# Kernel optimization log

Hardware: AMD Instinct MI355X
Metric: run time of the kernel (lower is better)

## Reference

```python
import jax, jax.numpy as jnp
import numpy as np

B_SZ = 16
IN_CH = 4
OUT_CH = 256          # d_model
KSIZE = 16
STRIDE = 8
L_IN = 20000
D_STATE = 128
EXPAND = 2
D_INNER = EXPAND * OUT_CH            # 512
HEADDIM = 64
NHEADS = D_INNER // HEADDIM          # 8
D_CONV = 4
NGROUPS = 1
L_CONV = (L_IN - KSIZE) // STRIDE + 1  # 2499
FLAT = STRIDE * L_CONV                 # 19992 == Config.INPUT_LENGTH
CHUNK = 128
DN = ('NCH', 'OIH', 'NCH')


def setup_inputs() -> dict:
    key = jax.random.key(0)
    ks = jax.random.split(key, 20)
    r = lambda i, shape, s=0.02: jax.random.normal(ks[i], shape, jnp.float32) * s
    return {
        'x': jax.random.normal(ks[0], (B_SZ, IN_CH, L_IN), jnp.float32),
        'conv_w': r(1, (OUT_CH, IN_CH, KSIZE), 0.1),
        'conv_b': r(2, (OUT_CH,), 0.1),
        'bn_w': jnp.ones((OUT_CH,), jnp.float32),
        'bn_b': jnp.zeros((OUT_CH,), jnp.float32),
        'in_proj_w': r(3, (2 * D_INNER + 2 * NGROUPS * D_STATE + NHEADS, OUT_CH)),
        'conv1d_w': r(4, (D_INNER + 2 * NGROUPS * D_STATE, 1, D_CONV), 0.2),
        'conv1d_b': r(5, (D_INNER + 2 * NGROUPS * D_STATE,), 0.1),
        'dt_bias': jnp.linspace(-4.0, -1.0, NHEADS, dtype=jnp.float32),
        'A_log': jnp.log(jnp.arange(1, NHEADS + 1, dtype=jnp.float32)),
        'D': r(6, (NHEADS,), 0.5) + 1.0,
        'norm_w': jnp.ones((D_INNER,), jnp.float32),
        'out_proj_w': r(7, (OUT_CH, D_INNER)),
        'conv1_w': r(8, (STRIDE, OUT_CH, KSIZE), 0.05),
        'conv1_b': r(9, (STRIDE,), 0.1),
        'w1': r(10, (512, FLAT)), 'b1': jnp.zeros((512,), jnp.float32),
        'w2': r(11, (256, 512), 0.05), 'b2': jnp.zeros((256,), jnp.float32),
        'w3': r(12, (64, 256), 0.05), 'b3': jnp.zeros((64,), jnp.float32),
        'w4': r(13, (1, 64), 0.05), 'b4': jnp.zeros((1,), jnp.float32),
    }


def _segsum(a):
    # a: [..., q] -> [..., q, q]; entry (i,j) = sum_{k=j+1..i} a_k on lower triangle
    q = a.shape[-1]
    cs = jnp.cumsum(a, axis=-1)
    seg = cs[..., :, None] - cs[..., None, :]
    mask = jnp.tril(jnp.ones((q, q), dtype=bool))
    return jnp.where(mask, seg, -jnp.inf)


def _ssd(xw, dA, Bm, Cm, chunk):
    # Chunked SSD (Mamba2): xw = dt-weighted inputs [b,l,h,p]; dA = dt*A [b,l,h];
    # Bm, Cm: [b,l,n]. Causal; zero-padding at the tail cannot affect y[:, :l].
    b, l, h, p = xw.shape
    n = Bm.shape[-1]
    pad = (-l) % chunk
    xw = jnp.pad(xw, ((0, 0), (0, pad), (0, 0), (0, 0)))
    dA = jnp.pad(dA, ((0, 0), (0, pad), (0, 0)))
    Bm = jnp.pad(Bm, ((0, 0), (0, pad), (0, 0)))
    Cm = jnp.pad(Cm, ((0, 0), (0, pad), (0, 0)))
    c = (l + pad) // chunk
    xw = xw.reshape(b, c, chunk, h, p)
    dA = dA.reshape(b, c, chunk, h).transpose(0, 3, 1, 2)   # [b,h,c,q]
    Bm = Bm.reshape(b, c, chunk, n)
    Cm = Cm.reshape(b, c, chunk, n)
    Acs = jnp.cumsum(dA, axis=-1)                            # [b,h,c,q]
    Ldiag = jnp.exp(_segsum(dA))                             # [b,h,c,q,q]
    Ydiag = jnp.einsum('bcln,bcsn,bhcls,bcshp->bclhp', Cm, Bm, Ldiag, xw)
    decay_states = jnp.exp(Acs[..., -1:] - Acs)              # [b,h,c,q]
    states = jnp.einsum('bcln,bhcl,bclhp->bchpn', Bm, decay_states, xw)
    chunk_decay = jnp.exp(Acs[..., -1])                      # [b,h,c]

    def step(carry, inp):
        s, d = inp
        return carry * d[..., None, None] + s, carry

    init = jnp.zeros((b, h, p, n), xw.dtype)
    _, prev = jax.lax.scan(step, init,
                           (states.transpose(1, 0, 2, 3, 4),
                            chunk_decay.transpose(2, 0, 1)))
    prev = prev.transpose(1, 0, 2, 3, 4)                     # [b,c,h,p,n]
    Yoff = jnp.einsum('bcln,bchpn,bhcl->bclhp', Cm, prev, jnp.exp(Acs))
    return (Ydiag + Yoff).reshape(b, l + pad, h, p)[:, :l]


def reference(x, conv_w, conv_b, bn_w, bn_b, in_proj_w, conv1d_w, conv1d_b,
              dt_bias, A_log, D, norm_w, out_proj_w, conv1_w, conv1_b,
              w1, b1, w2, b2, w3, b3, w4, b4):
    # conv -> BN (batch stats, training-mode math) -> ReLU
    h = jax.lax.conv_general_dilated(x, conv_w, (STRIDE,), 'VALID',
                                     dimension_numbers=DN) + conv_b[None, :, None]
    mean = h.mean(axis=(0, 2), keepdims=True)
    var = h.var(axis=(0, 2), keepdims=True)
    h = (h - mean) * jax.lax.rsqrt(var + 1e-5)
    h = jax.nn.relu(h * bn_w[None, :, None] + bn_b[None, :, None])
    u = h.transpose(0, 2, 1)                                 # [b, l, d_model]

    # ---- Mamba2 block ----
    zxbcdt = u @ in_proj_w.T                                 # [b, l, 1288]
    z, xBC, dt = jnp.split(zxbcdt, [D_INNER, 2 * D_INNER + 2 * NGROUPS * D_STATE], axis=-1)
    # causal depthwise conv1d over xBC + SiLU
    xBC_t = jnp.pad(xBC.transpose(0, 2, 1), ((0, 0), (0, 0), (D_CONV - 1, 0)))
    xBC_t = jax.lax.conv_general_dilated(xBC_t, conv1d_w, (1,), 'VALID',
                                         dimension_numbers=DN,
                                         feature_group_count=xBC.shape[-1])
    xBC = jax.nn.silu((xBC_t + conv1d_b[None, :, None]).transpose(0, 2, 1))
    xm, Bm, Cm = jnp.split(xBC, [D_INNER, D_INNER + NGROUPS * D_STATE], axis=-1)
    dt = jax.nn.softplus(dt + dt_bias)                       # [b, l, nheads]
    A = -jnp.exp(A_log)                                      # [nheads]
    xh = xm.reshape(xm.shape[0], xm.shape[1], NHEADS, HEADDIM)
    y = _ssd(xh * dt[..., None], dt * A, Bm, Cm, CHUNK)
    y = y + D[None, None, :, None] * xh                      # D skip
    y = y.reshape(y.shape[0], y.shape[1], D_INNER)
    # gated RMSNorm (norm_before_gate=False): rmsnorm(y * silu(z)) * w
    y = y * jax.nn.silu(z)
    y = y * jax.lax.rsqrt(jnp.mean(y * y, axis=-1, keepdims=True) + 1e-5) * norm_w
    y = y @ out_proj_w.T                                     # [b, l, d_model]

    # conv1 with padding='same' (PyTorch: left=(k-1)//2, right=k-1-left)
    h = y.transpose(0, 2, 1)
    pad_l = (KSIZE - 1) // 2
    h = jax.lax.conv_general_dilated(h, conv1_w, (1,), [(pad_l, KSIZE - 1 - pad_l)],
                                     dimension_numbers=DN) + conv1_b[None, :, None]
    f = h.reshape(h.shape[0], -1)                            # [b, 8*2499=19992]
    f = jax.nn.relu(f @ w1.T + b1)
    f = jax.nn.relu(f @ w2.T + b2)
    f = jax.nn.relu(f @ w3.T + b3)
    return f @ w4.T + b4                                     # [b, 1]
```

## Files before the change

kernel.cpp:

```cpp
#include <hip/hip_runtime.h>
#include <math.h>

constexpr int B    = 16;
constexpr int L    = 2499;
constexpr int DIN  = 512;
constexpr int NH   = 8;
constexpr int DS   = 128;
constexpr int NC   = 20;
constexpr int XBCD = 768;
constexpr int FLAT = 19992;
constexpr long ROWS = (long)B * L;

constexpr size_t S_DTV  = 0;
constexpr size_t S_CS   = 1279488;
constexpr size_t S_STAT = 2590208;
constexpr size_t S_WPK  = 2594304;
constexpr size_t S_HALO = 2725376;
constexpr size_t OFF_HT  = 4199936;
constexpr size_t OFF_XBC = 24671744;
constexpr size_t OFF_CBST= 86087168;
constexpr size_t CB_OFF  = 0;
constexpr size_t ST_OFF  = 5242880;
constexpr size_t Z_OFF   = 0;
constexpr size_t F_OFF   = 0;
constexpr size_t O1_OFF  = 1279488;
constexpr size_t O2_OFF  = 1312256;
constexpr size_t O3_OFF  = 1328640;
constexpr size_t WS_NEEDED = 127030784;

typedef unsigned short u16;
typedef __attribute__((ext_vector_type(8))) short bf16x8;
typedef __attribute__((ext_vector_type(4))) float f32x4;

__device__ __forceinline__ float bf2f(unsigned int u) {
    return __uint_as_float(u << 16);
}
__device__ __forceinline__ u16 f2bf(float f) {
    unsigned int x = __float_as_uint(f);
    unsigned int r = x + 0x7fffu + ((x >> 16) & 1u);
    return (u16)(r >> 16);
}
__device__ __forceinline__ unsigned int pk2(float a, float b) {
    return (unsigned int)f2bf(a) | ((unsigned int)f2bf(b) << 16);
}
__device__ __forceinline__ void ld8bf(const u16* p, float* o) {
    uint4 v = *(const uint4*)p;
    o[0]=bf2f(v.x&0xffffu); o[1]=bf2f(v.x>>16);
    o[2]=bf2f(v.y&0xffffu); o[3]=bf2f(v.y>>16);
    o[4]=bf2f(v.z&0xffffu); o[5]=bf2f(v.z>>16);
    o[6]=bf2f(v.w&0xffffu); o[7]=bf2f(v.w>>16);
}
__device__ __forceinline__ void ld4bf(const u16* p, float* o) {
    uint2 v = *(const uint2*)p;
    o[0]=bf2f(v.x&0xffffu); o[1]=bf2f(v.x>>16);
    o[2]=bf2f(v.y&0xffffu); o[3]=bf2f(v.y>>16);
}
__device__ __forceinline__ void st8bf(u16* p, const float* s) {
    uint4 v;
    v.x = pk2(s[0],s[1]); v.y = pk2(s[2],s[3]);
    v.z = pk2(s[4],s[5]); v.w = pk2(s[6],s[7]);
    *(uint4*)p = v;
}
__device__ __forceinline__ float siluf(float x) { return x / (1.f + expf(-x)); }

__global__ __launch_bounds__(256) void k_zero(float* __restrict__ p, int n) {
    int i = blockIdx.x * 256 + threadIdx.x;
    if (i < n) p[i] = 0.f;
}

__global__ __launch_bounds__(256) void k_wcvt(const float* __restrict__ src,
                                              u16* __restrict__ dst, int n) {
    int i = blockIdx.x * 256 + threadIdx.x;
    if (i < n) dst[i] = f2bf(src[i]);
}

template <bool IM2COL, bool BF16OUT>
__global__ __launch_bounds__(256) void gemm_mfma(const void* __restrict__ Ap,
                                                 const u16* __restrict__ Wb,
                                                 void* __restrict__ Cp,
                                                 int M, int N, int K, int lda, int ldc) {
    __shared__ u16 Als[128 * 40];
    __shared__ u16 Bls[128 * 40];
    int tid = threadIdx.x;
    int wave = tid >> 6, lane = tid & 63;
    int wr = wave >> 1, wc = wave & 1;
    int m0 = blockIdx.x * 128, n0 = blockIdx.y * 128;
    int l15 = lane & 15, l4 = lane >> 4;
    int srow = tid >> 1, scol = (tid & 1) * 16;

    f32x4 acc[4][4];
    #pragma unroll
    for (int i = 0; i < 4; ++i)
        #pragma unroll
        for (int j = 0; j < 4; ++j)
            acc[i][j] = (f32x4){0.f, 0.f, 0.f, 0.f};

    for (int k0 = 0; k0 < K; k0 += 32) {
        {
            int am = m0 + srow;
            uint4 v0 = {0,0,0,0}, v1 = {0,0,0,0};
            if (am < M) {
                if (IM2COL) {
                    const float* x = (const float*)Ap;
                    int b = am / L, l = am - b * L;
                    int ic = (k0 + scol) >> 4;
                    const float* px = x + ((long)(b * 4 + ic)) * 20000 + l * 8;
                    float4 f0 = *(const float4*)(px);
                    float4 f1 = *(const float4*)(px + 4);
                    float4 f2 = *(const float4*)(px + 8);
                    float4 f3 = *(const float4*)(px + 12);
                    v0.x = pk2(f0.x,f0.y); v0.y = pk2(f0.z,f0.w);
                    v0.z = pk2(f1.x,f1.y); v0.w = pk2(f1.z,f1.w);
                    v1.x = pk2(f2.x,f2.y); v1.y = pk2(f2.z,f2.w);
                    v1.z = pk2(f3.x,f3.y); v1.w = pk2(f3.z,f3.w);
                } else {
                    const u16* pa = (const u16*)Ap + (long)am * lda + k0 + scol;
                    v0 = *(const uint4*)pa;
                    v1 = *(const uint4*)(pa + 8);
                }
            }
            *(uint4*)&Als[srow * 40 + scol]     = v0;
            *(uint4*)&Als[srow * 40 + scol + 8] = v1;
        }
        {
            const u16* pw = Wb + (long)(n0 + srow) * K + k0 + scol;
            *(uint4*)&Bls[srow * 40 + scol]     = *(const uint4*)pw;
            *(uint4*)&Bls[srow * 40 + scol + 8] = *(const uint4*)(pw + 8);
        }
        __syncthreads();

        bf16x8 af[4], bfr[4];
        #pragma unroll
        for (int i = 0; i < 4; ++i) {
            af[i]  = *(const bf16x8*)&Als[(wr * 64 + i * 16 + l15) * 40 + l4 * 8];
            bfr[i] = *(const bf16x8*)&Bls[(wc * 64 + i * 16 + l15) * 40 + l4 * 8];
        }
        #pragma unroll
        for (int i = 0; i < 4; ++i)
            #pragma unroll
            for (int j = 0; j < 4; ++j)
                acc[i][j] = __builtin_amdgcn_mfma_f32_16x16x32_bf16(
                    af[i], bfr[j], acc[i][j], 0, 0, 0);
        __syncthreads();
    }

    #pragma unroll
    for (int i = 0; i < 4; ++i) {
        #pragma unroll
        for (int j = 0; j < 4; ++j) {
            int n = n0 + wc * 64 + j * 16 + l15;
            #pragma unroll
            for (int r = 0; r < 4; ++r) {
                int m = m0 + wr * 64 + i * 16 + l4 * 4 + r;
                if (m < M) {
                    if (BF16OUT) ((u16*)Cp)[(long)m * ldc + n] = f2bf(acc[i][j][r]);
                    else         ((float*)Cp)[(long)m * ldc + n] = acc[i][j][r];
                }
            }
        }
    }
}

__global__ __launch_bounds__(256) void k_bnstats(const u16* __restrict__ h,
                                                 float* __restrict__ sums,
                                                 float* __restrict__ sumsq) {
    int c = threadIdx.x;
    float s = 0.f, s2 = 0.f;
    for (long r = blockIdx.x; r < ROWS; r += gridDim.x) {
        float v = bf2f(h[r * 256 + c]);
        s += v; s2 += v * v;
    }
    atomicAdd(&sums[c], s);
    atomicAdd(&sumsq[c], s2);
}

__global__ __launch_bounds__(256) void k_bnfinal(const float* __restrict__ sums,
                                                 const float* __restrict__ sumsq,
                                                 const float* __restrict__ bn_w,
                                                 const float* __restrict__ bn_b,
                                                 float* __restrict__ scale,
                                                 float* __restrict__ shift) {
    int c = threadIdx.x;
    float mean = sums[c] / (float)ROWS;
    float var  = sumsq[c] / (float)ROWS - mean * mean;
    float inv  = rsqrtf(var + 1e-5f);
    float sc   = bn_w[c] * inv;
    scale[c] = sc;
    shift[c] = bn_b[c] - mean * sc;
}

__global__ __launch_bounds__(256) void k_bnapply(u16* __restrict__ ht,
                                                 const float* __restrict__ scale,
                                                 const float* __restrict__ shift) {
    long i = ((long)blockIdx.x * 256 + threadIdx.x) * 8;
    int c = (int)(i & 255);
    float v[8];
    ld8bf(ht + i, v);
    float4 s0 = *(const float4*)(scale + c), s1 = *(const float4*)(scale + c + 4);
    float4 h0 = *(const float4*)(shift + c), h1 = *(const float4*)(shift + c + 4);
    v[0]=fmaxf(fmaf(v[0],s0.x,h0.x),0.f); v[1]=fmaxf(fmaf(v[1],s0.y,h0.y),0.f);
    v[2]=fmaxf(fmaf(v[2],s0.z,h0.z),0.f); v[3]=fmaxf(fmaf(v[3],s0.w,h0.w),0.f);
    v[4]=fmaxf(fmaf(v[4],s1.x,h1.x),0.f); v[5]=fmaxf(fmaf(v[5],s1.y,h1.y),0.f);
    v[6]=fmaxf(fmaf(v[6],s1.z,h1.z),0.f); v[7]=fmaxf(fmaf(v[7],s1.w,h1.w),0.f);
    st8bf(ht + i, v);
}

__global__ __launch_bounds__(256) void k_dtproj(const u16* __restrict__ u,
                                                const float* __restrict__ in_proj_w,
                                                const float* __restrict__ dt_bias,
                                                float* __restrict__ dtv) {
    long idx = (long)blockIdx.x * 256 + threadIdx.x;
    if (idx >= ROWS * 8) return;
    int h = (int)(idx & 7);
    long row = idx >> 3;
    const float* wr = in_proj_w + (long)(1280 + h) * 256;
    const u16* ar = u + row * 256;
    float acc = dt_bias[h];
    for (int k = 0; k < 256; ++k)
        acc = fmaf(bf2f(ar[k]), wr[k], acc);
    dtv[idx] = (acc > 20.f) ? acc : log1pf(expf(acc));
}

__global__ __launch_bounds__(256) void k_halo(const u16* __restrict__ xbc,
                                              u16* __restrict__ halo) {
    long idx = (long)blockIdx.x * 256 + threadIdx.x;
    if (idx >= 16L * 19 * 3 * 768) return;
    int ch = (int)(idx % 768);
    long t1 = idx / 768;
    int j = (int)(t1 % 3);
    long t2 = t1 / 3;
    int t = (int)(t2 % 19) + 1;
    int b = (int)(t2 / 19);
    halo[(((long)b * 20 + t) * 3 + j) * 768 + ch] =
        xbc[((long)b * L + t * 128 - 3 + j) * 768 + ch];
}

__global__ __launch_bounds__(256) void k_dwip(u16* __restrict__ xbc,
                                              const u16* __restrict__ halo,
                                              const float* __restrict__ w,
                                              const float* __restrict__ bias) {
    int cg = blockIdx.x % 3;
    int t  = (blockIdx.x / 3) % 20;
    int b  = blockIdx.x / 60;
    int ch = cg * 256 + threadIdx.x;
    int l0 = t * 128, l1 = min(l0 + 128, L);
    float W0 = w[ch*4+0], W1 = w[ch*4+1], W2 = w[ch*4+2], W3 = w[ch*4+3];
    float bs = bias[ch];
    float p0 = 0.f, p1 = 0.f, p2 = 0.f;
    if (t > 0) {
        const u16* hp = halo + (((long)b * 20 + t) * 3) * 768 + ch;
        p0 = bf2f(hp[0]); p1 = bf2f(hp[768]); p2 = bf2f(hp[1536]);
    }
    u16* base = xbc + ((long)b * L + l0) * 768 + ch;
    for (int l = l0; l < l1; ++l) {
        float p3 = bf2f(*base);
        float acc = fmaf(p0, W0, fmaf(p1, W1, fmaf(p2, W2, fmaf(p3, W3, bs))));
        *base = f2bf(siluf(acc));
        p0 = p1; p1 = p2; p2 = p3;
        base += 768;
    }
}

__global__ __launch_bounds__(128) void k_cs(const float* __restrict__ dtv,
                                            const float* __restrict__ A_log,
                                            float* __restrict__ cs) {
    int c = blockIdx.x % NC;
    int h = (blockIdx.x / NC) % NH;
    int b = blockIdx.x / (NC * NH);
    int q = threadIdx.x;
    int lg = c * 128 + q;
    float Av = -expf(A_log[h]);
    float dA = 0.f;
    if (lg < L) dA = dtv[((long)b * L + lg) * 8 + h] * Av;
    __shared__ float buf[128];
    buf[q] = dA;
    __syncthreads();
    for (int off = 1; off < 128; off <<= 1) {
        float add = (q >= off) ? buf[q - off] : 0.f;
        __syncthreads();
        buf[q] += add;
        __syncthreads();
    }
    cs[(long)blockIdx.x * 128 + q] = buf[q];
}

__global__ __launch_bounds__(256) void k_cb(const u16* __restrict__ xbc,
                                            u16* __restrict__ cb, int bo) {
    int c = blockIdx.x % NC, bl = blockIdx.x / NC;
    int b = bo + bl;
    long bcl = blockIdx.x;
    __shared__ u16 Als[128 * 40];
    __shared__ u16 Bls[128 * 40];
    int tid = threadIdx.x;
    int wave = tid >> 6, lane = tid & 63;
    int wr = wave >> 1, wc = wave & 1;
    int l15 = lane & 15, l4 = lane >> 4;
    int srow = tid >> 1, scol = (tid & 1) * 16;

    f32x4 acc[4][4];
    #pragma unroll
    for (int i = 0; i < 4; ++i)
        #pragma unroll
        for (int j = 0; j < 4; ++j)
            acc[i][j] = (f32x4){0.f, 0.f, 0.f, 0.f};

    int lg = c * 128 + srow;
    const u16* prow = xbc + ((long)b * L + lg) * XBCD;

    for (int k0 = 0; k0 < 128; k0 += 32) {
        uint4 cv0 = {0,0,0,0}, cv1 = cv0, bv0 = cv0, bv1 = cv0;
        if (lg < L) {
            cv0 = *(const uint4*)(prow + 640 + k0 + scol);
            cv1 = *(const uint4*)(prow + 640 + k0 + scol + 8);
            bv0 = *(const uint4*)(prow + 512 + k0 + scol);
            bv1 = *(const uint4*)(prow + 512 + k0 + scol + 8);
        }
        *(uint4*)&Als[srow * 40 + scol]     = cv0;
        *(uint4*)&Als[srow * 40 + scol + 8] = cv1;
        *(uint4*)&Bls[srow * 40 + scol]     = bv0;
        *(uint4*)&Bls[srow * 40 + scol + 8] = bv1;
        __syncthreads();

        bf16x8 af[4], bfr[4];
        #pragma unroll
        for (int i = 0; i < 4; ++i) {
            af[i]  = *(const bf16x8*)&Als[(wr * 64 + i * 16 + l15) * 40 + l4 * 8];
            bfr[i] = *(const bf16x8*)&Bls[(wc * 64 + i * 16 + l15) * 40 + l4 * 8];
        }
        #pragma unroll
        for (int i = 0; i < 4; ++i)
            #pragma unroll
            for (int j = 0; j < 4; ++j)
                acc[i][j] = __builtin_amdgcn_mfma_f32_16x16x32_bf16(
                    af[i], bfr[j], acc[i][j], 0, 0, 0);
        __syncthreads();
    }

    #pragma unroll
    for (int i = 0; i < 4; ++i)
        #pragma unroll
        for (int j = 0; j < 4; ++j) {
            int n = wc * 64 + j * 16 + l15;
            #pragma unroll
            for (int r = 0; r < 4; ++r) {
                int m = wr * 64 + i * 16 + l4 * 4 + r;
                cb[(bcl * 128 + m) * 128 + n] = f2bf(acc[i][j][r]);
            }
        }
}

__global__ __launch_bounds__(256) void k_states(const u16* __restrict__ xbc,
                                                const float* __restrict__ dtv,
                                                const float* __restrict__ cs,
                                                u16* __restrict__ st, int bo) {
    int h = blockIdx.x & 7;
    int c = (blockIdx.x >> 3) % NC;
    int bl = blockIdx.x / (8 * NC);
    int b = bo + bl;
    __shared__ u16 At[128][136];
    __shared__ u16 Bt[64][136];
    long csbase = (((long)b * 8 + h) * NC + c) * 128;
    float csLast = cs[csbase + 127];
    int tid = threadIdx.x;
    int lane = tid & 63, wave = tid >> 6;
    int wr = wave >> 1, wc = wave & 1;
    int l15 = lane & 15, l4 = lane >> 4;

    int l0 = 2 * (tid & 63), l1 = l0 + 1;
    int q = tid >> 6;
    int lg0 = c * 128 + l0, lg1 = c * 128 + l1;
    long row0 = (long)b * L + lg0, row1 = row0 + 1;
    float wl0 = 0.f, wl1 = 0.f, dt0 = 0.f, dt1 = 0.f;
    if (lg0 < L) { wl0 = expf(csLast - cs[csbase + l0]); dt0 = dtv[row0 * 8 + h]; }
    if (lg1 < L) { wl1 = expf(csLast - cs[csbase + l1]); dt1 = dtv[row1 * 8 + h]; }

    #pragma unroll
    for (int nb = 0; nb < 4; ++nb) {
        int n0 = q * 32 + nb * 8;
        float a0[8] = {0,0,0,0,0,0,0,0}, a1[8] = {0,0,0,0,0,0,0,0};
        if (lg0 < L) ld8bf(xbc + row0 * XBCD + 512 + n0, a0);
        if (lg1 < L) ld8bf(xbc + row1 * XBCD + 512 + n0, a1);
        #pragma unroll
        for (int i = 0; i < 8; ++i)
            *(unsigned int*)&At[n0 + i][l0] = pk2(a0[i] * wl0, a1[i] * wl1);
    }
    #pragma unroll
    for (int pb = 0; pb < 2; ++pb) {
        int p0 = q * 16 + pb * 8;
        float a0[8] = {0,0,0,0,0,0,0,0}, a1[8] = {0,0,0,0,0,0,0,0};
        if (lg0 < L) ld8bf(xbc + row0 * XBCD + h * 64 + p0, a0);
        if (lg1 < L) ld8bf(xbc + row1 * XBCD + h * 64 + p0, a1);
        #pragma unroll
        for (int i = 0; i < 8; ++i)
            *(unsigned int*)&Bt[p0 + i][l0] = pk2(a0[i] * dt0, a1[i] * dt1);
    }
    __syncthreads();

    f32x4 acc[4][2];
    #pragma unroll
    for (int i = 0; i < 4; ++i)
        #pragma unroll
        for (int j = 0; j < 2; ++j)
            acc[i][j] = (f32x4){0.f, 0.f, 0.f, 0.f};

    #pragma unroll
    for (int k0 = 0; k0 < 128; k0 += 32) {
        bf16x8 af[4], bfr[2];
        #pragma unroll
        for (int i = 0; i < 4; ++i)
            af[i] = *(const bf16x8*)&At[wr * 64 + i * 16 + l15][k0 + l4 * 8];
        #pragma unroll
        for (int j = 0; j < 2; ++j)
            bfr[j] = *(const bf16x8*)&Bt[wc * 32 + j * 16 + l15][k0 + l4 * 8];
        #pragma unroll
        for (int i = 0; i < 4; ++i)
            #pragma unroll
            for (int j = 0; j < 2; ++j)
                acc[i][j] = __builtin_amdgcn_mfma_f32_16x16x32_bf16(
                    af[i], bfr[j], acc[i][j], 0, 0, 0);
    }

    long basep = (long)blockIdx.x * 8192;
    #pragma unroll
    for (int i = 0; i < 4; ++i)
        #pragma unroll
        for (int j = 0; j < 2; ++j) {
            int p = wc * 32 + j * 16 + l15;
            #pragma unroll
            for (int r = 0; r < 4; ++r) {
                int n = wr * 64 + i * 16 + l4 * 4 + r;
                st[basep + n * 64 + p] = f2bf(acc[i][j][r]);
            }
        }
}

__global__ __launch_bounds__(256) void k_scan(const float* __restrict__ cs,
                                              u16* __restrict__ st, int bo) {
    int h = blockIdx.x & 7, bl = blockIdx.x >> 3;
    int b = bo + bl;
    int tid = threadIdx.x;
    float carry[32];
    #pragma unroll
    for (int i = 0; i < 32; ++i) carry[i] = 0.f;
    long csbase = ((long)b * 8 + h) * NC * 128;
    for (int c = 0; c < NC; ++c) {
        float cd = expf(cs[csbase + c * 128 + 127]);
        u16* p = st + (((long)bl * NC + c) * 8 + h) * 8192;
        #pragma unroll
        for (int i = 0; i < 32; ++i) {
            int e = tid + i * 256;
            float v = bf2f(p[e]);
            p[e] = f2bf(carry[i]);
            carry[i] = carry[i] * cd + v;
        }
    }
}

__global__ __launch_bounds__(256) void k_yout(u16* __restrict__ xbc,
                                              const float* __restrict__ dtv,
                                              const float* __restrict__ cs,
                                              const u16* __restrict__ cb,
                                              const u16* __restrict__ st,
                                              const float* __restrict__ Dv, int bo) {
    int h = blockIdx.x & 7;
    int c = (blockIdx.x >> 3) % NC;
    int bl = blockIdx.x / (8 * NC);
    int b = bo + bl;
    long bcl = (long)bl * NC + c;
    __shared__ u16 Am[128][136];
    __shared__ u16 Bt[64][136];
    __shared__ float csb[128], ecs[128];
    int tid = threadIdx.x;
    long csbase = (((long)b * 8 + h) * NC + c) * 128;
    if (tid < 128) {
        float v = cs[csbase + tid];
        csb[tid] = v;
        ecs[tid] = expf(v);
    }
    __syncthreads();

    int lane = tid & 63, wave = tid >> 6;
    int wr = wave >> 1, wc = wave & 1;
    int l15 = lane & 15, l4 = lane >> 4;
    int lrow = tid >> 1, sh = (tid & 1) * 64;
    int l0 = 2 * (tid & 63), l1 = l0 + 1;
    int q = tid >> 6;
    int lg0 = c * 128 + l0, lg1 = c * 128 + l1;
    long row0 = (long)b * L + lg0, row1 = row0 + 1;

    {
        float cl = csb[lrow];
        const u16* cbrow = cb + (bcl * 128 + lrow) * 128;
        #pragma unroll
        for (int sb = 0; sb < 8; ++sb) {
            int s0 = sh + sb * 8;
            float a[8];
            ld8bf(cbrow + s0, a);
            #pragma unroll
            for (int i = 0; i < 8; ++i) {
                int s = s0 + i;
                float w = (s <= lrow) ? expf(cl - csb[s]) : 0.f;
                a[i] *= w;
            }
            st8bf(&Am[lrow][s0], a);
        }
        float dt0 = 0.f, dt1 = 0.f;
        if (lg0 < L) dt0 = dtv[row0 * 8 + h];
        if (lg1 < L) dt1 = dtv[row1 * 8 + h];
        #pragma unroll
        for (int pb = 0; pb < 2; ++pb) {
            int p0 = q * 16 + pb * 8;
            float a0[8] = {0,0,0,0,0,0,0,0}, a1[8] = {0,0,0,0,0,0,0,0};
            if (lg0 < L) ld8bf(xbc + row0 * XBCD + h * 64 + p0, a0);
            if (lg1 < L) ld8bf(xbc + row1 * XBCD + h * 64 + p0, a1);
            #pragma unroll
            for (int i = 0; i < 8; ++i)
                *(unsigned int*)&Bt[p0 + i][l0] = pk2(a0[i] * dt0, a1[i] * dt1);
        }
    }
    __syncthreads();

    f32x4 acc[4][2];
    #pragma unroll
    for (int i = 0; i < 4; ++i)
        #pragma unroll
        for (int j = 0; j < 2; ++j)
            acc[i][j] = (f32x4){0.f, 0.f, 0.f, 0.f};

    #pragma unroll
    for (int k0 = 0; k0 < 128; k0 += 32) {
        bf16x8 af[4], bfr[2];
        #pragma unroll
        for (int i = 0; i < 4; ++i)
            af[i] = *(const bf16x8*)&Am[wr * 64 + i * 16 + l15][k0 + l4 * 8];
        #pragma unroll
        for (int j = 0; j < 2; ++j)
            bfr[j] = *(const bf16x8*)&Bt[wc * 32 + j * 16 + l15][k0 + l4 * 8];
        #pragma unroll
        for (int i = 0; i < 4; ++i)
            #pragma unroll
            for (int j = 0; j < 2; ++j)
                acc[i][j] = __builtin_amdgcn_mfma_f32_16x16x32_bf16(
                    af[i], bfr[j], acc[i][j], 0, 0, 0);
    }
    __syncthreads();

    {
        float el = ecs[lrow];
        int lgr = c * 128 + lrow;
        const u16* xr = xbc + ((long)b * L + lgr) * XBCD + 640;
        #pragma unroll
        for (int nb = 0; nb < 8; ++nb) {
            int n0 = sh + nb * 8;
            float a[8] = {0,0,0,0,0,0,0,0};
            if (lgr < L) {
                ld8bf(xr + n0, a);
                #pragma unroll
                for (int i = 0; i < 8; ++i) a[i] *= el;
            }
            st8bf(&Am[lrow][n0], a);
        }
        const u16* pv = st + (bcl * 8 + h) * 8192;
        #pragma unroll
        for (int pb = 0; pb < 2; ++pb) {
            int p0 = q * 16 + pb * 8;
            float a0[8], a1[8];
            ld8bf(pv + (long)l0 * 64 + p0, a0);
            ld8bf(pv + (long)l1 * 64 + p0, a1);
            #pragma unroll
            for (int i = 0; i < 8; ++i)
                *(unsigned int*)&Bt[p0 + i][l0] = pk2(a0[i], a1[i]);
        }
    }
    __syncthreads();

    #pragma unroll
    for (int k0 = 0; k0 < 128; k0 += 32) {
        bf16x8 af[4], bfr[2];
        #pragma unroll
        for (int i = 0; i < 4; ++i)
            af[i] = *(const bf16x8*)&Am[wr * 64 + i * 16 + l15][k0 + l4 * 8];
        #pragma unroll
        for (int j = 0; j < 2; ++j)
            bfr[j] = *(const bf16x8*)&Bt[wc * 32 + j * 16 + l15][k0 + l4 * 8];
        #pragma unroll
        for (int i = 0; i < 4; ++i)
            #pragma unroll
            for (int j = 0; j < 2; ++j)
                acc[i][j] = __builtin_amdgcn_mfma_f32_16x16x32_bf16(
                    af[i], bfr[j], acc[i][j], 0, 0, 0);
    }

    float Dh = Dv[h];
    #pragma unroll
    for (int i = 0; i < 4; ++i)
        #pragma unroll
        for (int r = 0; r < 4; ++r) {
            int l = wr * 64 + i * 16 + l4 * 4 + r;
            int lg = c * 128 + l;
            if (lg >= L) continue;
            long row = (long)b * L + lg;
            #pragma unroll
            for (int j = 0; j < 2; ++j) {
                int p = wc * 32 + j * 16 + l15;
                u16* xp = xbc + row * XBCD + h * 64 + p;
                float xv = bf2f(*xp);
                *xp = f2bf(fmaf(Dh, xv, acc[i][j][r]));
            }
        }
}

__global__ __launch_bounds__(256) void k_rmsnorm(u16* __restrict__ y,
                                                 const u16* __restrict__ z,
                                                 const float* __restrict__ nw) {
    long r = blockIdx.x;
    int tid = threadIdx.x;
    float v0 = bf2f(y[r * XBCD + tid]), v1 = bf2f(y[r * XBCD + 256 + tid]);
    float z0 = bf2f(z[r * DIN + tid]),  z1 = bf2f(z[r * DIN + 256 + tid]);
    v0 *= siluf(z0);
    v1 *= siluf(z1);
    __shared__ float red[256];
    red[tid] = v0 * v0 + v1 * v1;
    __syncthreads();
    for (int s = 128; s > 0; s >>= 1) {
        if (tid < s) red[tid] += red[tid + s];
        __syncthreads();
    }
    float sc = rsqrtf(red[0] / 512.f + 1e-5f);
    y[r * XBCD + tid]       = f2bf(v0 * sc * nw[tid]);
    y[r * XBCD + 256 + tid] = f2bf(v1 * sc * nw[256 + tid]);
}

__global__ __launch_bounds__(256) void k_wpack(const float* __restrict__ w,
                                               u16* __restrict__ wp) {
    int idx = blockIdx.x * 256 + threadIdx.x;
    if (idx >= 8 * 256 * 16) return;
    int k = idx & 15;
    int cidx = (idx >> 4) & 255;
    int s = idx >> 12;
    wp[(s * 16 + k) * 256 + cidx] = f2bf(w[idx]);
}

__global__ __launch_bounds__(256) void k_conv1(const float* __restrict__ G,
                                               const float* __restrict__ bias,
                                               float* __restrict__ f) {
    long idx = (long)blockIdx.x * 256 + threadIdx.x;
    if (idx >= (long)B * 8 * L) return;
    int l = (int)(idx % L);
    long t = idx / L;
    int s = (int)(t & 7);
    int b = (int)(t >> 3);
    float acc = bias[s];
    #pragma unroll
    for (int k = 0; k < 16; ++k) {
        int ls = l + k - 7;
        if (ls >= 0 && ls < L)
            acc += G[((long)b * L + ls) * 128 + s * 16 + k];
    }
    f[(long)b * FLAT + s * L + l] = acc;
}

__global__ __launch_bounds__(256) void k_mlp1(const float* __restrict__ f,
                                              const float* __restrict__ w1,
                                              const float* __restrict__ b1,
                                              float* __restrict__ out1) {
    int n = blockIdx.x;
    int tid = threadIdx.x;
    float acc[16];
    #pragma unroll
    for (int i = 0; i < 16; ++i) acc[i] = 0.f;
    const float* wr = w1 + (long)n * FLAT;
    for (int k = tid; k < FLAT; k += 256) {
        float wv = wr[k];
        #pragma unroll
        for (int b = 0; b < 16; ++b) acc[b] = fmaf(wv, f[(long)b * FLAT + k], acc[b]);
    }
    __shared__ float red[16][257];
    #pragma unroll
    for (int b = 0; b < 16; ++b) red[b][tid] = acc[b];
    __syncthreads();
    for (int s = 128; s > 0; s >>= 1) {
        if (tid < s)
            #pragma unroll
            for (int b = 0; b < 16; ++b) red[b][tid] += red[b][tid + s];
        __syncthreads();
    }
    if (tid < 16) out1[(long)tid * 512 + n] = fmaxf(red[tid][0] + b1[n], 0.f);
}

__global__ __launch_bounds__(256) void k_mlp2(const float* __restrict__ in,
                                              const float* __restrict__ w,
                                              const float* __restrict__ bias,
                                              float* __restrict__ out) {
    int b = blockIdx.x, n = threadIdx.x;
    const float* ir = in + b * 512;
    const float* wr = w + (long)n * 512;
    float acc = 0.f;
    for (int k = 0; k < 512; ++k) acc = fmaf(ir[k], wr[k], acc);
    out[b * 256 + n] = fmaxf(acc + bias[n], 0.f);
}

__global__ __launch_bounds__(64) void k_mlp3(const float* __restrict__ in,
                                             const float* __restrict__ w,
                                             const float* __restrict__ bias,
                                             float* __restrict__ out) {
    int b = blockIdx.x, n = threadIdx.x;
    const float* ir = in + b * 256;
    const float* wr = w + (long)n * 256;
    float acc = 0.f;
    for (int k = 0; k < 256; ++k) acc = fmaf(ir[k], wr[k], acc);
    out[b * 64 + n] = fmaxf(acc + bias[n], 0.f);
}

__global__ __launch_bounds__(64) void k_mlp4(const float* __restrict__ in,
                                             const float* __restrict__ w4,
                                             const float* __restrict__ b4,
                                             float* __restrict__ dout) {
    int b = blockIdx.x, k = threadIdx.x;
    float v = in[b * 64 + k] * w4[k];
    #pragma unroll
    for (int off = 32; off > 0; off >>= 1) v += __shfl_down(v, off);
    if (k == 0) dout[b] = v + b4[0];
}

extern "C" void kernel_launch(void* const* d_in, const int* in_sizes, int n_in,
                              void* d_out, int out_size, void* d_ws, size_t ws_size,
                              hipStream_t stream) {
    (void)in_sizes; (void)n_in; (void)out_size;
    if (ws_size < WS_NEEDED) return;

    const float* x         = (const float*)d_in[0];
    const float* conv_w    = (const float*)d_in[1];
    const float* bn_w      = (const float*)d_in[3];
    const float* bn_b      = (const float*)d_in[4];
    const float* in_proj_w = (const float*)d_in[5];
    const float* conv1d_w  = (const float*)d_in[6];
    const float* conv1d_b  = (const float*)d_in[7];
    const float* dt_bias   = (const float*)d_in[8];
    const float* A_log     = (const float*)d_in[9];
    const float* Dp        = (const float*)d_in[10];
    const float* norm_w    = (const float*)d_in[11];
    const float* out_proj_w= (const float*)d_in[12];
    const float* conv1_w   = (const float*)d_in[13];
    const float* conv1_b   = (const float*)d_in[14];
    const float* w1 = (const float*)d_in[15]; const float* b1 = (const float*)d_in[16];
    const float* w2 = (const float*)d_in[17]; const float* b2 = (const float*)d_in[18];
    const float* w3 = (const float*)d_in[19]; const float* b3 = (const float*)d_in[20];
    const float* w4 = (const float*)d_in[21]; const float* b4 = (const float*)d_in[22];

    char* base = (char*)d_ws;
    float* dtv  = (float*)(base + S_DTV);
    float* cs   = (float*)(base + S_CS);
    float* sums = (float*)(base + S_STAT);
    float* sumsq= sums + 256;
    float* scale= sums + 512;
    float* shift= sums + 768;
    u16*   cwbf = (u16*)(base + S_WPK);
    u16*   wbf  = (u16*)(base + S_HALO);
    u16*   halo = (u16*)(base + S_HALO);
    u16*   ht   = (u16*)(base + OFF_HT);
    u16*   xbc  = (u16*)(base + OFF_XBC);
    u16*   cb   = (u16*)(base + OFF_CBST + CB_OFF);
    u16*   st   = (u16*)(base + OFF_CBST + ST_OFF);
    u16*   zb   = (u16*)(base + OFF_CBST + Z_OFF);
    float* G    = (float*)(base + OFF_XBC);
    float* fbuf = (float*)(base + OFF_CBST + F_OFF);
    float* o1   = (float*)(base + OFF_CBST + O1_OFF);
    float* o2   = (float*)(base + OFF_CBST + O2_OFF);
    float* o3   = (float*)(base + OFF_CBST + O3_OFF);
    u16*   yproj= ht;

    k_wcvt<<<64, 256, 0, stream>>>(conv_w, cwbf, 256 * 64);
    gemm_mfma<true, true><<<dim3(313, 2), 256, 0, stream>>>(
        x, cwbf, ht, (int)ROWS, 256, 64, 0, 256);

    k_zero<<<2, 256, 0, stream>>>(sums, 512);
    k_bnstats<<<256, 256, 0, stream>>>(ht, sums, sumsq);
    k_bnfinal<<<1, 256, 0, stream>>>(sums, sumsq, bn_w, bn_b, scale, shift);
    k_bnapply<<<4998, 256, 0, stream>>>(ht, scale, shift);

    k_wcvt<<<768, 256, 0, stream>>>(in_proj_w + 512L * 256, wbf, 768 * 256);
    gemm_mfma<false, true><<<dim3(313, 6), 256, 0, stream>>>(
        ht, wbf, xbc, (int)ROWS, 768, 256, 256, 768);
    k_dtproj<<<1250, 256, 0, stream>>>(ht, in_proj_w, dt_bias, dtv);

    k_halo<<<2736, 256, 0, stream>>>(xbc, halo);
    k_dwip<<<960, 256, 0, stream>>>(xbc, halo, conv1d_w, conv1d_b);
    k_cs<<<2560, 128, 0, stream>>>(dtv, A_log, cs);

    for (int bh = 0; bh < 2; ++bh) {
        int bo = bh * 8;
        k_cb<<<160, 256, 0, stream>>>(xbc, cb, bo);
        k_states<<<1280, 256, 0, stream>>>(xbc, dtv, cs, st, bo);
        k_scan<<<64, 256, 0, stream>>>(cs, st, bo);
        k_yout<<<1280, 256, 0, stream>>>(xbc, dtv, cs, cb, st, Dp, bo);
    }

    k_wcvt<<<512, 256, 0, stream>>>(in_proj_w, wbf, 512 * 256);
    gemm_mfma<false, true><<<dim3(313, 4), 256, 0, stream>>>(
        ht, wbf, zb, (int)ROWS, 512, 256, 256, 512);

    k_rmsnorm<<<39984, 256, 0, stream>>>(xbc, zb, norm_w);
    k_wcvt<<<512, 256, 0, stream>>>(out_proj_w, wbf, 256 * 512);
    gemm_mfma<false, true><<<dim3(313, 2), 256, 0, stream>>>(
        xbc, wbf, yproj, (int)ROWS, 256, 512, 768, 256);

    k_wpack<<<128, 256, 0, stream>>>(conv1_w, wbf);
    gemm_mfma<false, false><<<dim3(313, 1), 256, 0, stream>>>(
        yproj, wbf, G, (int)ROWS, 128, 256, 256, 128);
    k_conv1<<<1250, 256, 0, stream>>>(G, conv1_b, fbuf);

    k_mlp1<<<512, 256, 0, stream>>>(fbuf, w1, b1, o1);
    k_mlp2<<<16, 256, 0, stream>>>(o1, w2, b2, o2);
    k_mlp3<<<16, 64, 0, stream>>>(o2, w3, b3, o3);
    k_mlp4<<<16, 64, 0, stream>>>(o3, w4, b4, (float*)d_out);
}
```

Measured before the change: 769.0 us.

## Run first MLP layer on bf16 MFMA with split-K atomics; widen scan grid

Replaces the scalar fp32 k_mlp1 reduction with a bf16 MFMA kernel over a padded w1 copy and bf16 activations. K is split into 25 slices that accumulate into an fp32 buffer with atomics, followed by a bias+ReLU finalize kernel. The conv1 GEMM output G and conv1 activations move to bf16, and k_scan is split four ways across the state to raise parallelism. This adds a per-call w1 conversion pass (about 20 MB read) and costs precision from bf16 activations and weights in the large dot product.

```diff
diff --git a/kernel.cpp b/kernel.cpp
--- a/kernel.cpp
+++ b/kernel.cpp
@@ -9,6 +9,7 @@
 constexpr int NC   = 20;
 constexpr int XBCD = 768;
 constexpr int FLAT = 19992;
+constexpr int FLATP= 20000;
 constexpr long ROWS = (long)B * L;
 
 constexpr size_t S_DTV  = 0;
@@ -23,9 +24,11 @@
 constexpr size_t ST_OFF  = 5242880;
 constexpr size_t Z_OFF   = 0;
 constexpr size_t F_OFF   = 0;
-constexpr size_t O1_OFF  = 1279488;
-constexpr size_t O2_OFF  = 1312256;
-constexpr size_t O3_OFF  = 1328640;
+constexpr size_t O1A_OFF = 640000;
+constexpr size_t O1_OFF  = 672768;
+constexpr size_t O2_OFF  = 705536;
+constexpr size_t O3_OFF  = 721920;
+constexpr size_t W1B_OFF = 726016;
 constexpr size_t WS_NEEDED = 127030784;
 
 typedef unsigned short u16;
@@ -72,6 +75,24 @@
                                               u16* __restrict__ dst, int n) {
     int i = blockIdx.x * 256 + threadIdx.x;
     if (i < n) dst[i] = f2bf(src[i]);
+}
+
+__global__ __launch_bounds__(256) void k_w1cvt(const float* __restrict__ w1,
+                                               u16* __restrict__ w1b) {
+    long e0 = ((long)blockIdx.x * 256 + threadIdx.x) * 8;
+    int n = (int)(e0 / FLATP);
+    int k = (int)(e0 - (long)n * FLATP);
+    const float* src = w1 + (long)n * FLAT + k;
+    u16* dst = w1b + e0;
+    if (k + 8 <= FLAT) {
+        float4 a = *(const float4*)src;
+        float4 b = *(const float4*)(src + 4);
+        *(uint4*)dst = (uint4){pk2(a.x,a.y), pk2(a.z,a.w), pk2(b.x,b.y), pk2(b.z,b.w)};
+    } else {
+        #pragma unroll
+        for (int i = 0; i < 8; ++i)
+            dst[i] = (k + i < FLAT) ? f2bf(src[i]) : (u16)0;
+    }
 }
 
 template <bool IM2COL, bool BF16OUT>
@@ -436,18 +457,18 @@
 
 __global__ __launch_bounds__(256) void k_scan(const float* __restrict__ cs,
                                               u16* __restrict__ st, int bo) {
-    int h = blockIdx.x & 7, bl = blockIdx.x >> 3;
+    int h = blockIdx.x & 7, bl = (blockIdx.x >> 3) & 7, q = blockIdx.x >> 6;
     int b = bo + bl;
     int tid = threadIdx.x;
-    float carry[32];
-    #pragma unroll
-    for (int i = 0; i < 32; ++i) carry[i] = 0.f;
+    float carry[8];
+    #pragma unroll
+    for (int i = 0; i < 8; ++i) carry[i] = 0.f;
     long csbase = ((long)b * 8 + h) * NC * 128;
     for (int c = 0; c < NC; ++c) {
         float cd = expf(cs[csbase + c * 128 + 127]);
-        u16* p = st + (((long)bl * NC + c) * 8 + h) * 8192;
-        #pragma unroll
-        for (int i = 0; i < 32; ++i) {
+        u16* p = st + (((long)bl * NC + c) * 8 + h) * 8192 + q * 2048;
+        #pragma unroll
+        for (int i = 0; i < 8; ++i) {
             int e = tid + i * 256;
             float v = bf2f(p[e]);
             p[e] = f2bf(carry[i]);
@@ -641,11 +662,16 @@
     wp[(s * 16 + k) * 256 + cidx] = f2bf(w[idx]);
 }
 
-__global__ __launch_bounds__(256) void k_conv1(const float* __restrict__ G,
+__global__ __launch_bounds__(256) void k_conv1(const u16* __restrict__ G,
                                                const float* __restrict__ bias,
-                                               float* __restrict__ f) {
+                                               u16* __restrict__ f) {
     long idx = (long)blockIdx.x * 256 + threadIdx.x;
-    if (idx >= (long)B * 8 * L) return;
+    if (idx >= (long)B * 8 * L) {
+        long j = idx - (long)B * 8 * L;
+        if (j < 16 * 8)
+            f[(j >> 3) * FLATP + FLAT + (j & 7)] = 0;
+        return;
+    }
     int l = (int)(idx % L);
     long t = idx / L;
     int s = (int)(t & 7);
@@ -655,37 +681,40 @@
     for (int k = 0; k < 16; ++k) {
         int ls = l + k - 7;
         if (ls >= 0 && ls < L)
-            acc += G[((long)b * L + ls) * 128 + s * 16 + k];
-    }
-    f[(long)b * FLAT + s * L + l] = acc;
-}
-
-__global__ __launch_bounds__(256) void k_mlp1(const float* __restrict__ f,
-                                              const float* __restrict__ w1,
-                                              const float* __restrict__ b1,
-                                              float* __restrict__ out1) {
-    int n = blockIdx.x;
-    int tid = threadIdx.x;
-    float acc[16];
-    #pragma unroll
-    for (int i = 0; i < 16; ++i) acc[i] = 0.f;
-    const float* wr = w1 + (long)n * FLAT;
-    for (int k = tid; k < FLAT; k += 256) {
-        float wv = wr[k];
-        #pragma unroll
-        for (int b = 0; b < 16; ++b) acc[b] = fmaf(wv, f[(long)b * FLAT + k], acc[b]);
-    }
-    __shared__ float red[16][257];
-    #pragma unroll
-    for (int b = 0; b < 16; ++b) red[b][tid] = acc[b];
-    __syncthreads();
-    for (int s = 128; s > 0; s >>= 1) {
-        if (tid < s)
-            #pragma unroll
-            for (int b = 0; b < 16; ++b) red[b][tid] += red[b][tid + s];
-        __syncthreads();
-    }
-    if (tid < 16) out1[(long)tid * 512 + n] = fmaxf(red[tid][0] + b1[n], 0.f);
+            acc += bf2f(G[((long)b * L + ls) * 128 + s * 16 + k]);
+    }
+    f[(long)b * FLATP + s * L + l] = f2bf(acc);
+}
+
+__global__ __launch_bounds__(256) void k_mlp1(const u16* __restrict__ fb,
+                                              const u16* __restrict__ w1b,
+                                              float* __restrict__ o1acc) {
+    int wave = threadIdx.x >> 6, lane = threadIdx.x & 63;
+    int l15 = lane & 15, l4 = lane >> 4;
+    int n0 = blockIdx.x * 64 + wave * 16;
+    int k0 = blockIdx.y * 800;
+    const u16* fp = fb + (long)l15 * FLATP + k0 + l4 * 8;
+    const u16* wp = w1b + (long)(n0 + l15) * FLATP + k0 + l4 * 8;
+    f32x4 acc = (f32x4){0.f, 0.f, 0.f, 0.f};
+    #pragma unroll
+    for (int kk = 0; kk < 25; ++kk) {
+        bf16x8 af = *(const bf16x8*)fp;
+        bf16x8 bf = *(const bf16x8*)wp;
+        acc = __builtin_amdgcn_mfma_f32_16x16x32_bf16(af, bf, acc, 0, 0, 0);
+        fp += 32; wp += 32;
+    }
+    #pragma unroll
+    for (int r = 0; r < 4; ++r) {
+        int b = l4 * 4 + r;
+        atomicAdd(&o1acc[b * 512 + n0 + l15], acc[r]);
+    }
+}
+
+__global__ __launch_bounds__(256) void k_mlp1fin(const float* __restrict__ o1acc,
+                                                 const float* __restrict__ b1,
+                                                 float* __restrict__ o1) {
+    int i = blockIdx.x * 256 + threadIdx.x;
+    o1[i] = fmaxf(o1acc[i] + b1[i & 511], 0.f);
 }
 
 __global__ __launch_bounds__(256) void k_mlp2(const float* __restrict__ in,
@@ -763,11 +792,13 @@
     u16*   cb   = (u16*)(base + OFF_CBST + CB_OFF);
     u16*   st   = (u16*)(base + OFF_CBST + ST_OFF);
     u16*   zb   = (u16*)(base + OFF_CBST + Z_OFF);
-    float* G    = (float*)(base + OFF_XBC);
-    float* fbuf = (float*)(base + OFF_CBST + F_OFF);
+    u16*   G    = (u16*)(base + OFF_XBC);
+    u16*   fbuf = (u16*)(base + OFF_CBST + F_OFF);
+    float* o1a  = (float*)(base + OFF_CBST + O1A_OFF);
     float* o1   = (float*)(base + OFF_CBST + O1_OFF);
     float* o2   = (float*)(base + OFF_CBST + O2_OFF);
     float* o3   = (float*)(base + OFF_CBST + O3_OFF);
+    u16*   w1b  = (u16*)(base + OFF_CBST + W1B_OFF);
     u16*   yproj= ht;
 
     k_wcvt<<<64, 256, 0, stream>>>(conv_w, cwbf, 256 * 64);
@@ -792,7 +823,7 @@
         int bo = bh * 8;
         k_cb<<<160, 256, 0, stream>>>(xbc, cb, bo);
         k_states<<<1280, 256, 0, stream>>>(xbc, dtv, cs, st, bo);
-        k_scan<<<64, 256, 0, stream>>>(cs, st, bo);
+        k_scan<<<256, 256, 0, stream>>>(cs, st, bo);
         k_yout<<<1280, 256, 0, stream>>>(xbc, dtv, cs, cb, st, Dp, bo);
     }
 
@@ -806,11 +837,14 @@
         xbc, wbf, yproj, (int)ROWS, 256, 512, 768, 256);
 
     k_wpack<<<128, 256, 0, stream>>>(conv1_w, wbf);
-    gemm_mfma<false, false><<<dim3(313, 1), 256, 0, stream>>>(
+    gemm_mfma<false, true><<<dim3(313, 1), 256, 0, stream>>>(
         yproj, wbf, G, (int)ROWS, 128, 256, 256, 128);
     k_conv1<<<1250, 256, 0, stream>>>(G, conv1_b, fbuf);
 
-    k_mlp1<<<512, 256, 0, stream>>>(fbuf, w1, b1, o1);
+    k_w1cvt<<<5000, 256, 0, stream>>>(w1, w1b);
+    k_zero<<<32, 256, 0, stream>>>(o1a, 8192);
+    k_mlp1<<<dim3(8, 25), 256, 0, stream>>>(fbuf, w1b, o1a);
+    k_mlp1fin<<<32, 256, 0, stream>>>(o1a, b1, o1);
     k_mlp2<<<16, 256, 0, stream>>>(o1, w2, b2, o2);
     k_mlp3<<<16, 64, 0, stream>>>(o2, w3, b3, o3);
     k_mlp4<<<16, 64, 0, stream>>>(o3, w4, b4, (float*)d_out);
```

New measurement: 709.9 us. 7.7% less time.
